# Kernel tuning notes

Measured on AMD Instinct MI355X. Metric: run time of the kernel, lower is better.

The kernel has to match this reference:

```python
import jax, jax.numpy as jnp
import numpy as np

HEADS = 8
DIM_HEAD = 64
NUM_MEM_KV = 4
DIM = 512
B, H, W = 16, 32, 32


def setup_inputs() -> dict:
    key = jax.random.key(0)
    k1, k2, k3, k4 = jax.random.split(key, 4)
    hidden = HEADS * DIM_HEAD
    x = jax.random.normal(k1, (B, DIM, H, W), dtype=jnp.float32)
    gamma = jnp.zeros((DIM,), dtype=jnp.float32)  # nn.Parameter init zeros
    mem_kv = jax.random.normal(k2, (2, HEADS, NUM_MEM_KV, DIM_HEAD), dtype=jnp.float32)
    w_qkv = jax.random.normal(k3, (3 * hidden, DIM), dtype=jnp.float32) * (1.0 / np.sqrt(DIM))
    w_out = jax.random.normal(k4, (DIM, hidden), dtype=jnp.float32) * (1.0 / np.sqrt(hidden))
    return {"x": x, "gamma": gamma, "mem_kv": mem_kv, "w_qkv": w_qkv, "w_out": w_out}


def reference(x, gamma, mem_kv, w_qkv, w_out):
    b, c, h, w = x.shape
    n = h * w
    # RMSNorm: F.normalize over channel dim, then * (gamma+1) * sqrt(dim)
    denom = jnp.maximum(jnp.linalg.norm(x, axis=1, keepdims=True), 1e-12)
    xn = (x / denom) * (gamma[None, :, None, None] + 1.0) * (c ** 0.5)
    # 1x1 conv qkv projection
    qkv = jnp.einsum('bchw,oc->bohw', xn, w_qkv)  # [b, 3*hidden, h, w]
    q, k, v = jnp.split(qkv, 3, axis=1)

    def to_heads(t):
        # 'b (h c) x y -> b h (x y) c'
        return t.reshape(b, HEADS, DIM_HEAD, n).transpose(0, 1, 3, 2)

    q = to_heads(q) * (DIM_HEAD ** -0.5)  # [b, heads, n, d]
    k = to_heads(k)
    v = to_heads(v)
    mk = jnp.broadcast_to(mem_kv[0], (b, HEADS, NUM_MEM_KV, DIM_HEAD))
    mv = jnp.broadcast_to(mem_kv[1], (b, HEADS, NUM_MEM_KV, DIM_HEAD))
    k = jnp.concatenate([mk, k], axis=2)  # [b, heads, m+n, d]
    v = jnp.concatenate([mv, v], axis=2)
    sim = jnp.einsum('bhid,bhjd->bhij', q, k)
    attn = jax.nn.softmax(sim, axis=-1)
    out = jnp.einsum('bhij,bhjd->bhid', attn, v)  # [b, heads, n, d]
    # 'b h (x y) d -> b (h d) x y'
    out = out.transpose(0, 1, 3, 2).reshape(b, HEADS * DIM_HEAD, h, w)
    return jnp.einsum('bchw,oc->bohw', out, w_out)
```

## Files before the change

kernel.cpp:

```cpp
#include <hip/hip_runtime.h>
#include <cstdint>
#include <cstddef>

constexpr int kHeads = 8;
constexpr int kDHead = 64;
constexpr int kC     = 512;
constexpr int kB     = 16;
constexpr int kN     = 1024;
constexpr int kHid   = 512;

typedef _Float16 h16;
typedef _Float16 h8 __attribute__((ext_vector_type(8)));
typedef _Float16 h4 __attribute__((ext_vector_type(4)));
typedef _Float16 h2 __attribute__((ext_vector_type(2)));
typedef float f32x4 __attribute__((ext_vector_type(4)));

__global__ __launch_bounds__(256) void rms_transpose_kernel(
    const float* __restrict__ x, h16* __restrict__ xh)
{
  __shared__ float T[64 * 64];
  __shared__ float red[4][64];
  __shared__ float sl[64];
  const int t  = threadIdx.x;
  const int b  = blockIdx.x >> 4;
  const int p0 = (blockIdx.x & 15) << 6;
  const float* xb = x + (size_t)b * kC * kN + p0;

  const int pix = t & 63, sub = t >> 6;
  float sum = 0.f;
  #pragma unroll 8
  for (int c = sub * 128; c < sub * 128 + 128; ++c) {
    const float v = xb[(size_t)c * kN + pix];
    sum = fmaf(v, v, sum);
  }
  red[sub][pix] = sum;
  __syncthreads();
  if (t < 64) {
    const float tot = red[0][t] + red[1][t] + red[2][t] + red[3][t];
    sl[t] = 22.62741699796952f / fmaxf(sqrtf(tot), 1e-12f);
  }
  __syncthreads();

  for (int cc = 0; cc < 8; cc++) {
    const int c0 = cc * 64;
    #pragma unroll
    for (int i = 0; i < 4; i++) {
      const int r  = i * 16 + (t >> 4);
      const int pg = t & 15;
      const float4 v = *(const float4*)(xb + (size_t)(c0 + r) * kN + pg * 4);
      *(float4*)&T[r * 64 + ((pg ^ (r & 15)) << 2)] = v;
    }
    __syncthreads();
    #pragma unroll
    for (int i2 = 0; i2 < 2; i2++) {
      const int p  = i2 * 32 + (t >> 3);
      const int cg = t & 7;
      const float sc = sl[p];
      h16 hv[8];
      #pragma unroll
      for (int j = 0; j < 8; j++) {
        const int c = cg * 8 + j;
        const float v = T[c * 64 + (((p >> 2) ^ (c & 15)) << 2) + (p & 3)];
        hv[j] = (h16)(v * sc);
      }
      *(h8*)&xh[((size_t)b * kN + p0 + p) * kC + c0 + cg * 8] = *(h8*)hv;
    }
    __syncthreads();
  }
}

__global__ __launch_bounds__(64) void prep_w_kernel(
    const float* __restrict__ w_qkv, const float* __restrict__ gamma,
    const float* __restrict__ w_out, h16* __restrict__ wqh,
    h16* __restrict__ wouth)
{
  const int row = blockIdx.x;
  const int c0  = threadIdx.x * 8;
  if (row < 1536) {
    const float sc = (row < 512) ? 0.125f * 1.4426950408889634f : 1.f;
    const float4 a  = *(const float4*)(w_qkv + (size_t)row * kC + c0);
    const float4 b  = *(const float4*)(w_qkv + (size_t)row * kC + c0 + 4);
    const float4 g0 = *(const float4*)(gamma + c0);
    const float4 g1 = *(const float4*)(gamma + c0 + 4);
    h8 hv = { (h16)(a.x * (g0.x + 1.f) * sc), (h16)(a.y * (g0.y + 1.f) * sc),
              (h16)(a.z * (g0.z + 1.f) * sc), (h16)(a.w * (g0.w + 1.f) * sc),
              (h16)(b.x * (g1.x + 1.f) * sc), (h16)(b.y * (g1.y + 1.f) * sc),
              (h16)(b.z * (g1.z + 1.f) * sc), (h16)(b.w * (g1.w + 1.f) * sc) };
    *(h8*)&wqh[(size_t)row * kC + c0] = hv;
  } else {
    const int r = row - 1536;
    const float4 a = *(const float4*)(w_out + (size_t)r * kC + c0);
    const float4 b = *(const float4*)(w_out + (size_t)r * kC + c0 + 4);
    h8 hv = { (h16)a.x, (h16)a.y, (h16)a.z, (h16)a.w,
              (h16)b.x, (h16)b.y, (h16)b.z, (h16)b.w };
    *(h8*)&wouth[(size_t)r * kC + c0] = hv;
  }
}

__device__ __forceinline__ void gemm_loop_f16(
    const h16* __restrict__ Ag, const h16* __restrict__ Bg,
    h16 (*__restrict__ As)[8192], h16 (*__restrict__ Bs)[8192],
    int t, int w, int g, int lo, f32x4 (&acc)[4][4])
{
  const int wo = (w >> 1) * 64, wp = (w & 1) * 64;
  h8 stA[4], stB[4];
  auto load = [&](int kt) {
    const int k0 = kt * 64;
    #pragma unroll
    for (int i = 0; i < 4; i++) {
      const int f = t + i * 256, r = f >> 3, cg = f & 7;
      stA[i] = *(const h8*)(Ag + (size_t)r * kC + k0 + cg * 8);
      stB[i] = *(const h8*)(Bg + (size_t)r * kC + k0 + cg * 8);
    }
  };
  auto store = [&](int buf) {
    #pragma unroll
    for (int i = 0; i < 4; i++) {
      const int f = t + i * 256, r = f >> 3, cg = f & 7;
      const int off = r * 64 + ((cg ^ (r & 7)) << 3);
      *(h8*)&As[buf][off] = stA[i];
      *(h8*)&Bs[buf][off] = stB[i];
    }
  };
  load(0); store(0); __syncthreads();
  int buf = 0;
  for (int kt = 0; kt < 8; kt++) {
    if (kt < 7) load(kt + 1);
    h8 bfr[4][2];
    #pragma unroll
    for (int ni = 0; ni < 4; ni++) {
      const int row = wp + ni * 16 + lo;
      #pragma unroll
      for (int kb = 0; kb < 2; kb++)
        bfr[ni][kb] = *(const h8*)&Bs[buf][row * 64 + (((kb * 4 + g) ^ (row & 7)) << 3)];
    }
    #pragma unroll
    for (int mi = 0; mi < 4; mi++) {
      const int row = wo + mi * 16 + lo;
      const h8 a0 = *(const h8*)&As[buf][row * 64 + (((    g) ^ (row & 7)) << 3)];
      const h8 a1 = *(const h8*)&As[buf][row * 64 + (((4 + g) ^ (row & 7)) << 3)];
      #pragma unroll
      for (int ni = 0; ni < 4; ni++) {
        acc[mi][ni] = __builtin_amdgcn_mfma_f32_16x16x32_f16(a0, bfr[ni][0], acc[mi][ni], 0, 0, 0);
        acc[mi][ni] = __builtin_amdgcn_mfma_f32_16x16x32_f16(a1, bfr[ni][1], acc[mi][ni], 0, 0, 0);
      }
    }
    if (kt < 7) store(buf ^ 1);
    __syncthreads();
    buf ^= 1;
  }
}

__global__ __launch_bounds__(256) void qkv_mfma_kernel(
    const h16* __restrict__ xh, const h16* __restrict__ wqh,
    h16* __restrict__ Qh, h16* __restrict__ Kh, h16* __restrict__ VTh)
{
  __shared__ h16 As[2][8192];
  __shared__ h16 Bs[2][8192];
  const int t = threadIdx.x, lane = t & 63, w = t >> 6, g = lane >> 4, lo = lane & 15;
  const int o0 = blockIdx.x * 128;
  const int p0 = blockIdx.y * 128;
  const int b  = blockIdx.z;
  const h16* Ag = wqh + (size_t)o0 * kC;
  const h16* Bg = xh + ((size_t)b * kN + p0) * kC;

  f32x4 acc[4][4];
  #pragma unroll
  for (int mi = 0; mi < 4; mi++)
    #pragma unroll
    for (int ni = 0; ni < 4; ni++) { f32x4 z = {0.f, 0.f, 0.f, 0.f}; acc[mi][ni] = z; }

  gemm_loop_f16(Ag, Bg, As, Bs, t, w, g, lo, acc);

  const int o_wave = o0 + (w >> 1) * 64;
  const int which  = o_wave >> 9;
  const int head   = (o_wave >> 6) & 7;
  const size_t bh  = (size_t)b * kHeads + head;
  const int pglob  = p0 + (w & 1) * 64;

  if (which == 2) {
    h16* Vdst = VTh + bh * (size_t)(kN * kDHead);
    #pragma unroll
    for (int mi = 0; mi < 4; mi++)
      #pragma unroll
      for (int ni = 0; ni < 4; ni++) {
        const int p = pglob + ni * 16 + lo;
        #pragma unroll
        for (int r = 0; r < 4; r++) {
          const int d = mi * 16 + g * 4 + r;
          Vdst[(size_t)d * kN + p] = (h16)((const float*)&acc[mi][ni])[r];
        }
      }
  } else {
    h16* lw = &As[0][0] + w * 4096;
    #pragma unroll
    for (int mi = 0; mi < 4; mi++) {
      const int gran0 = mi * 2 + (g >> 1);
      const int off   = (g & 1) * 4;
      #pragma unroll
      for (int ni = 0; ni < 4; ni++) {
        const int p = ni * 16 + lo;
        h4 pv = { (h16)acc[mi][ni].x, (h16)acc[mi][ni].y,
                  (h16)acc[mi][ni].z, (h16)acc[mi][ni].w };
        *(h4*)&lw[p * 64 + ((gran0 ^ (p & 7)) << 3) + off] = pv;
      }
    }
    __syncthreads();
    h16* dst = (which ? Kh : Qh) + bh * (size_t)(kN * kDHead);
    #pragma unroll
    for (int i = 0; i < 8; i++) {
      const int p  = i * 8 + (lane >> 3);
      const int dg = lane & 7;
      const h8 v = *(const h8*)&lw[p * 64 + ((dg ^ (p & 7)) << 3)];
      *(h8*)&dst[((size_t)pglob + p) * kDHead + dg * 8] = v;
    }
  }
}

__global__ __launch_bounds__(256, 3) void attn_mfma_kernel(
    const h16* __restrict__ Qh, const h16* __restrict__ Kh,
    const h16* __restrict__ VTh, const float* __restrict__ mem_kv,
    h16* __restrict__ ah)
{
  __shared__ h16 Kl[2][4096];
  __shared__ h16 Vl[2][4096];

  const int t    = threadIdx.x;
  const int lane = t & 63;
  const int w    = t >> 6;
  const int g    = lane >> 4;
  const int lo   = lane & 15;
  const int id   = blockIdx.x;
  const int xcd  = id & 7;
  const int slot = id >> 3;
  const int grp  = xcd * 16 + (slot & 15);
  const int qt   = slot >> 4;
  const int h = grp & 7, b = grp >> 3;

  const h16* Qg = Qh  + (size_t)grp * 65536;
  const h16* Kg = Kh  + (size_t)grp * 65536;
  const h16* Vg = VTh + (size_t)grp * 65536;
  const int q0 = qt * 128 + w * 32;

  h8 qf[2][2];
  #pragma unroll
  for (int ni = 0; ni < 2; ni++)
    #pragma unroll
    for (int kb = 0; kb < 2; kb++)
      qf[ni][kb] = *(const h8*)(Qg + (size_t)(q0 + ni*16 + lo) * 64 + kb*32 + g*8);

  {
    const int kr = t >> 2, dq = (t & 3) << 4;
    h16 hv[16];
    if (kr < 4) {
      const float* src = mem_kv + (size_t)h * 256 + kr * 64 + dq;
      #pragma unroll
      for (int i = 0; i < 16; i++) hv[i] = (h16)src[i];
    } else {
      #pragma unroll
      for (int i = 0; i < 16; i++) hv[i] = (h16)0.f;
    }
    const int sw = (kr & 7) << 3;
    *(h8*)&Kl[0][kr*64 + ( dq      ^ sw)] = *(h8*)&hv[0];
    *(h8*)&Kl[0][kr*64 + ((dq + 8) ^ sw)] = *(h8*)&hv[8];

    const int d = t >> 2, kq = (t & 3) << 4;
    h16 vv[16];
    #pragma unroll
    for (int i = 0; i < 16; i++) vv[i] = (h16)0.f;
    if (kq == 0) {
      const float* src = mem_kv + 2048 + (size_t)h * 256 + d;
      #pragma unroll
      for (int i = 0; i < 4; i++) vv[i] = (h16)src[i * 64];
    }
    const int sv = (d & 7) << 3;
    *(h8*)&Vl[0][d*64 + ( kq      ^ sv)] = *(h8*)&vv[0];
    *(h8*)&Vl[0][d*64 + ((kq + 8) ^ sv)] = *(h8*)&vv[8];
  }
  __syncthreads();

  f32x4 o[2][4];
  #pragma unroll
  for (int qb = 0; qb < 2; qb++)
    #pragma unroll
    for (int db = 0; db < 4; db++) { f32x4 z = {0.f,0.f,0.f,0.f}; o[qb][db] = z; }
  float lst[2] = {0.f, 0.f};
  const f32x4 cinit = {-8.f, -8.f, -8.f, -8.f};

  h8 stK[2], stV[2];
  #pragma unroll 1
  for (int kt = 0; kt <= 16; kt++) {
    if (kt < 16) {
      const size_t key0 = (size_t)kt * 64;
      #pragma unroll
      for (int ps = 0; ps < 2; ps++) {
        const int f = t + ps*256, r = f >> 3, cb = (f & 7) << 3;
        stK[ps] = *(const h8*)(Kg + (key0 + r) * 64 + cb);
        stV[ps] = *(const h8*)(Vg + (size_t)r * 1024 + key0 + cb);
      }
    }
    const h16* KL = Kl[kt & 1];
    const h16* VL = Vl[kt & 1];

    f32x4 s[4][2];
    __builtin_amdgcn_s_setprio(1);
    #pragma unroll
    for (int mi = 0; mi < 4; mi++) {
      const int row = mi*16 + lo;
      const int sw = (row & 7) << 3;
      const h8 k0 = *(const h8*)&KL[row*64 + (( g*8)      ^ sw)];
      const h8 k1 = *(const h8*)&KL[row*64 + ((32 + g*8)  ^ sw)];
      #pragma unroll
      for (int ni = 0; ni < 2; ni++) {
        f32x4 acc = __builtin_amdgcn_mfma_f32_16x16x32_f16(k0, qf[ni][0], cinit, 0, 0, 0);
        acc = __builtin_amdgcn_mfma_f32_16x16x32_f16(k1, qf[ni][1], acc, 0, 0, 0);
        s[mi][ni] = acc;
      }
    }
    __builtin_amdgcn_s_setprio(0);

    h4 p4[4][2];
    #pragma unroll
    for (int ni = 0; ni < 2; ni++) {
      #pragma unroll
      for (int mi = 0; mi < 4; mi++) {
        const float px = exp2f(s[mi][ni].x);
        const float py = exp2f(s[mi][ni].y);
        const float pz = exp2f(s[mi][ni].z);
        const float pw = exp2f(s[mi][ni].w);
        lst[ni] += (px + py) + (pz + pw);
        const h2 a = __builtin_bit_cast(h2, __builtin_amdgcn_cvt_pkrtz(px, py));
        const h2 c = __builtin_bit_cast(h2, __builtin_amdgcn_cvt_pkrtz(pz, pw));
        p4[mi][ni] = __builtin_shufflevector(a, c, 0, 1, 2, 3);
      }
    }

    __builtin_amdgcn_s_setprio(1);
    #pragma unroll
    for (int db = 0; db < 4; db++) {
      const int d = db*16 + lo;
      const int sw = (d & 7) << 3;
      h4 v4[4];
      #pragma unroll
      for (int mi = 0; mi < 4; mi++)
        v4[mi] = *(const h4*)&VL[d*64 + ((mi*16 + (g>>1)*8) ^ sw) + (g&1)*4];
      const h8 vB0 = __builtin_shufflevector(v4[0], v4[1], 0, 1, 2, 3, 4, 5, 6, 7);
      const h8 vB1 = __builtin_shufflevector(v4[2], v4[3], 0, 1, 2, 3, 4, 5, 6, 7);
      #pragma unroll
      for (int qb = 0; qb < 2; qb++) {
        const h8 pA0 = __builtin_shufflevector(p4[0][qb], p4[1][qb], 0, 1, 2, 3, 4, 5, 6, 7);
        const h8 pA1 = __builtin_shufflevector(p4[2][qb], p4[3][qb], 0, 1, 2, 3, 4, 5, 6, 7);
        o[qb][db] = __builtin_amdgcn_mfma_f32_16x16x32_f16(pA0, vB0, o[qb][db], 0, 0, 0);
        o[qb][db] = __builtin_amdgcn_mfma_f32_16x16x32_f16(pA1, vB1, o[qb][db], 0, 0, 0);
      }
    }
    __builtin_amdgcn_s_setprio(0);

    if (kt < 16) {
      #pragma unroll
      for (int ps = 0; ps < 2; ps++) {
        const int f = t + ps*256, r = f >> 3, cb = (f & 7) << 3;
        const int sw = (r & 7) << 3;
        *(h8*)&Kl[(kt + 1) & 1][r*64 + (cb ^ sw)] = stK[ps];
        *(h8*)&Vl[(kt + 1) & 1][r*64 + (cb ^ sw)] = stV[ps];
      }
    }
    __syncthreads();
  }

  #pragma unroll
  for (int qb = 0; qb < 2; qb++) {
    float l = lst[qb];
    l += __shfl_xor(l, 16);
    l += __shfl_xor(l, 32);
    l -= 0.234375f;
    const float il = 1.f / l;
    const float i0 = __shfl(il, g*4 + 0);
    const float i1 = __shfl(il, g*4 + 1);
    const float i2 = __shfl(il, g*4 + 2);
    const float i3 = __shfl(il, g*4 + 3);
    const int qg = (b << 10) + q0 + qb*16 + g*4;
    #pragma unroll
    for (int db = 0; db < 4; db++) {
      const int c = h*64 + db*16 + lo;
      ah[(size_t)(qg + 0) * kHid + c] = (h16)(o[qb][db].x * i0);
      ah[(size_t)(qg + 1) * kHid + c] = (h16)(o[qb][db].y * i1);
      ah[(size_t)(qg + 2) * kHid + c] = (h16)(o[qb][db].z * i2);
      ah[(size_t)(qg + 3) * kHid + c] = (h16)(o[qb][db].w * i3);
    }
  }
}

__global__ __launch_bounds__(256) void out_mfma_kernel(
    const h16* __restrict__ ah, const h16* __restrict__ wouth,
    float* __restrict__ out)
{
  __shared__ h16 As[2][8192];
  __shared__ h16 Bs[2][8192];
  const int t = threadIdx.x, lane = t & 63, w = t >> 6, g = lane >> 4, lo = lane & 15;
  const int o0 = blockIdx.x * 128;
  const int p0 = blockIdx.y * 128;
  const int b  = blockIdx.z;
  const h16* Ag = wouth + (size_t)o0 * kC;
  const h16* Bg = ah + ((size_t)b * kN + p0) * kC;

  f32x4 acc[4][4];
  #pragma unroll
  for (int mi = 0; mi < 4; mi++)
    #pragma unroll
    for (int ni = 0; ni < 4; ni++) { f32x4 z = {0.f, 0.f, 0.f, 0.f}; acc[mi][ni] = z; }

  gemm_loop_f16(Ag, Bg, As, Bs, t, w, g, lo, acc);

  const int ow = o0 + (w >> 1) * 64;
  const int pw = p0 + (w & 1) * 64;
  #pragma unroll
  for (int mi = 0; mi < 4; mi++)
    #pragma unroll
    for (int ni = 0; ni < 4; ni++) {
      const int p = pw + ni * 16 + lo;
      #pragma unroll
      for (int r = 0; r < 4; r++) {
        const int oc = ow + mi * 16 + g * 4 + r;
        out[((size_t)b * kHid + oc) * kN + p] = ((const float*)&acc[mi][ni])[r];
      }
    }
}

extern "C" void kernel_launch(void* const* d_in, const int* in_sizes, int n_in,
                              void* d_out, int out_size, void* d_ws, size_t ws_size,
                              hipStream_t stream) {
  (void)in_sizes; (void)n_in; (void)out_size; (void)ws_size;
  const float* x      = (const float*)d_in[0];
  const float* gamma  = (const float*)d_in[1];
  const float* mem_kv = (const float*)d_in[2];
  const float* w_qkv  = (const float*)d_in[3];
  const float* w_out  = (const float*)d_in[4];
  float* out = (float*)d_out;

  h16* xh    = (h16*)d_ws;
  h16* Qh    = xh + (size_t)16777216;
  h16* Kh    = Qh + (size_t)8388608;
  h16* VTh   = Kh + (size_t)8388608;
  h16* ah    = VTh + (size_t)8388608;
  h16* wqh   = ah + (size_t)8388608;
  h16* wouth = wqh + (size_t)786432;

  rms_transpose_kernel<<<256, 256, 0, stream>>>(x, xh);
  prep_w_kernel<<<2048, 64, 0, stream>>>(w_qkv, gamma, w_out, wqh, wouth);
  qkv_mfma_kernel<<<dim3(12, 8, 16), 256, 0, stream>>>(xh, wqh, Qh, Kh, VTh);
  attn_mfma_kernel<<<1024, 256, 0, stream>>>(Qh, Kh, VTh, mem_kv, ah);
  out_mfma_kernel<<<dim3(4, 8, 16), 256, 0, stream>>>(ah, wouth, out);
}
```

Baseline: 150.9 us.

## Split RMS norm and transpose into separate kernels for more parallelism

The fused RMS-norm+transpose kernel, which ran 256 blocks each looping over 8 channel chunks, is split in two. One kernel computes per-pixel scales into workspace, and a second kernel with 2048 blocks transposes and scales one 64x64 tile each. The intent is to raise occupancy and memory-level parallelism on a GPU with many CUs. The cost is an extra launch and reading x twice from global memory (32 MB input), though the second read may partly hit cache.

```diff
diff --git a/kernel.cpp b/kernel.cpp
--- a/kernel.cpp
+++ b/kernel.cpp
@@ -15,57 +15,64 @@
 typedef _Float16 h2 __attribute__((ext_vector_type(2)));
 typedef float f32x4 __attribute__((ext_vector_type(4)));
 
-__global__ __launch_bounds__(256) void rms_transpose_kernel(
-    const float* __restrict__ x, h16* __restrict__ xh)
-{
-  __shared__ float T[64 * 64];
+__global__ __launch_bounds__(256) void rms_scale_kernel(
+    const float* __restrict__ x, float* __restrict__ s)
+{
   __shared__ float red[4][64];
-  __shared__ float sl[64];
-  const int t  = threadIdx.x;
-  const int b  = blockIdx.x >> 4;
-  const int p0 = (blockIdx.x & 15) << 6;
-  const float* xb = x + (size_t)b * kC * kN + p0;
-
-  const int pix = t & 63, sub = t >> 6;
+  const int t   = threadIdx.x;
+  const int pix = t & 63;
+  const int sub = t >> 6;
+  const int gp  = blockIdx.x * 64 + pix;
+  const int b   = gp >> 10;
+  const int pp  = gp & 1023;
+  const float* xb = x + (size_t)b * kC * kN + pp;
   float sum = 0.f;
   #pragma unroll 8
   for (int c = sub * 128; c < sub * 128 + 128; ++c) {
-    const float v = xb[(size_t)c * kN + pix];
+    float v = xb[(size_t)c * kN];
     sum = fmaf(v, v, sum);
   }
   red[sub][pix] = sum;
   __syncthreads();
   if (t < 64) {
-    const float tot = red[0][t] + red[1][t] + red[2][t] + red[3][t];
-    sl[t] = 22.62741699796952f / fmaxf(sqrtf(tot), 1e-12f);
+    float tot = red[0][pix] + red[1][pix] + red[2][pix] + red[3][pix];
+    float nrm = fmaxf(sqrtf(tot), 1e-12f);
+    s[gp] = 22.62741699796952f / nrm;
+  }
+}
+
+__global__ __launch_bounds__(256) void transpose_scale_kernel(
+    const float* __restrict__ x, const float* __restrict__ s,
+    h16* __restrict__ xh)
+{
+  __shared__ float T[64 * 64];
+  const int t  = threadIdx.x;
+  const int c0 = blockIdx.x * 64;
+  const int p0 = blockIdx.y * 64;
+  const int b  = blockIdx.z;
+  const float* xb = x + (size_t)b * kC * kN + p0;
+
+  #pragma unroll
+  for (int i = 0; i < 4; i++) {
+    const int r  = i * 16 + (t >> 4);
+    const int pg = t & 15;
+    const float4 v = *(const float4*)(xb + (size_t)(c0 + r) * kN + pg * 4);
+    *(float4*)&T[r * 64 + ((pg ^ (r & 15)) << 2)] = v;
   }
   __syncthreads();
-
-  for (int cc = 0; cc < 8; cc++) {
-    const int c0 = cc * 64;
-    #pragma unroll
-    for (int i = 0; i < 4; i++) {
-      const int r  = i * 16 + (t >> 4);
-      const int pg = t & 15;
-      const float4 v = *(const float4*)(xb + (size_t)(c0 + r) * kN + pg * 4);
-      *(float4*)&T[r * 64 + ((pg ^ (r & 15)) << 2)] = v;
-    }
-    __syncthreads();
-    #pragma unroll
-    for (int i2 = 0; i2 < 2; i2++) {
-      const int p  = i2 * 32 + (t >> 3);
-      const int cg = t & 7;
-      const float sc = sl[p];
-      h16 hv[8];
-      #pragma unroll
-      for (int j = 0; j < 8; j++) {
-        const int c = cg * 8 + j;
-        const float v = T[c * 64 + (((p >> 2) ^ (c & 15)) << 2) + (p & 3)];
-        hv[j] = (h16)(v * sc);
-      }
-      *(h8*)&xh[((size_t)b * kN + p0 + p) * kC + c0 + cg * 8] = *(h8*)hv;
-    }
-    __syncthreads();
+  #pragma unroll
+  for (int i2 = 0; i2 < 2; i2++) {
+    const int p  = i2 * 32 + (t >> 3);
+    const int cg = t & 7;
+    const float sc = s[(b << 10) + p0 + p];
+    h16 hv[8];
+    #pragma unroll
+    for (int j = 0; j < 8; j++) {
+      const int c = cg * 8 + j;
+      const float v = T[c * 64 + (((p >> 2) ^ (c & 15)) << 2) + (p & 3)];
+      hv[j] = (h16)(v * sc);
+    }
+    *(h8*)&xh[((size_t)b * kN + p0 + p) * kC + c0 + cg * 8] = *(h8*)hv;
   }
 }
 
@@ -438,7 +445,8 @@
   const float* w_out  = (const float*)d_in[4];
   float* out = (float*)d_out;
 
-  h16* xh    = (h16*)d_ws;
+  float* s_scale = (float*)d_ws;
+  h16* xh    = (h16*)(s_scale + 16384);
   h16* Qh    = xh + (size_t)16777216;
   h16* Kh    = Qh + (size_t)8388608;
   h16* VTh   = Kh + (size_t)8388608;
@@ -446,7 +454,8 @@
   h16* wqh   = ah + (size_t)8388608;
   h16* wouth = wqh + (size_t)786432;
 
-  rms_transpose_kernel<<<256, 256, 0, stream>>>(x, xh);
+  rms_scale_kernel<<<256, 256, 0, stream>>>(x, s_scale);
+  transpose_scale_kernel<<<dim3(8, 16, 16), 256, 0, stream>>>(x, s_scale, xh);
   prep_w_kernel<<<2048, 64, 0, stream>>>(w_qkv, gamma, w_out, wqh, wouth);
   qkv_mfma_kernel<<<dim3(12, 8, 16), 256, 0, stream>>>(xh, wqh, Qh, Kh, VTh);
   attn_mfma_kernel<<<1024, 256, 0, stream>>>(Qh, Kh, VTh, mem_kv, ah);
```

Result: no change. 151.4 us, median of 3 (+0.4%).
